# Optimization experiments

Measured on AMD Instinct MI355X. Metric: run time of the kernel, lower is better.

The kernel has to match this reference:

```python
import jax, jax.numpy as jnp
import numpy as np

T, H, F, E, K = 2048, 1024, 1024, 8, 2  # tokens, hidden, ffn, experts, top_k


def setup_inputs() -> dict:
    key = jax.random.key(0)
    k1, k2, k3, k4, k5 = jax.random.split(key, 5)
    hidden_states = jax.random.normal(k1, (T, H), dtype=jnp.float32)
    # router outputs: positive weights (renormalize=False in module, used as-is)
    topk_weights = jax.random.uniform(k2, (T, K), dtype=jnp.float32)
    topk_ids = jax.random.randint(k3, (T, K), 0, E, dtype=jnp.int32)
    # gate_up: (E, 2F, H) with first F rows = gate, last F rows = up
    gate_up_weight = jax.random.normal(k4, (E, 2 * F, H), dtype=jnp.float32) * 0.02
    # down: (E, H, F)
    down_weight = jax.random.normal(k5, (E, H, F), dtype=jnp.float32) * 0.02
    return {
        'hidden_states': hidden_states,
        'topk_weights': topk_weights,
        'topk_ids': topk_ids,
        'gate_up_weight': gate_up_weight,
        'down_weight': down_weight,
    }


def reference(hidden_states, topk_weights, topk_ids, gate_up_weight, down_weight):
    # Fused MoE: per selected expert, y = (silu(x@Wg^T) * (x@Wu^T)) @ Wd^T,
    # combined with router weights (renormalize=False).
    f = down_weight.shape[-1]
    # [T, E, 2F]: gate_up projection for every expert (dense ref for grouped GEMM)
    gu = jnp.einsum('th,eoh->teo', hidden_states, gate_up_weight)
    gate, up = gu[..., :f], gu[..., f:]
    act = jax.nn.silu(gate) * up                     # [T, E, F]
    y = jnp.einsum('tef,ehf->teh', act, down_weight)  # [T, E, H]
    # gather the top-k experts per token and combine
    y_sel = jnp.take_along_axis(y, topk_ids[:, :, None], axis=1)  # [T, K, H]
    out = jnp.sum(y_sel * topk_weights[:, :, None], axis=1)       # [T, H]
    return out.astype(hidden_states.dtype)
```

## Files before the change

kernel.cpp:

```cpp
#include <hip/hip_runtime.h>
#include <hip/hip_bf16.h>

#define T_TOK 2048
#define HID   1024
#define FF    1024
#define NEXP  8
#define TOPK  2
#define NPAIR (T_TOK*TOPK)

#define BM 128
#define BN 128
#define BK 32
#define MAX_MT 40
#define MAXROWS (MAX_MT*BM)

using bf16x8 = __attribute__((ext_vector_type(8))) __bf16;
using f32x4  = __attribute__((ext_vector_type(4))) float;

__device__ __forceinline__ unsigned short f2bf(float f) {
    unsigned int u = __float_as_uint(f);
    unsigned int r = (u + 0x7FFF + ((u >> 16) & 1)) >> 16;
    return (unsigned short)r;
}
__device__ __forceinline__ float bf2f(unsigned short s) {
    return __uint_as_float(((unsigned int)s) << 16);
}

__global__ void setup_kernel(const int* __restrict__ ids,
                             int* __restrict__ pair_pos,
                             int* __restrict__ meta) {
    __shared__ int cnt[NEXP], cnt2[NEXP], base[NEXP];
    int tid = threadIdx.x;
    if (tid < NEXP) { cnt[tid] = 0; cnt2[tid] = 0; }
    __syncthreads();
    for (int p = tid; p < NPAIR; p += 256) atomicAdd(&cnt[ids[p]], 1);
    __syncthreads();
    if (tid == 0) {
        int mt = 0;
        for (int e = 0; e < NEXP; e++) {
            meta[e] = mt;
            base[e] = mt * BM;
            mt += (cnt[e] + BM - 1) / BM;
        }
        meta[NEXP] = mt;
    }
    __syncthreads();
    for (int p = tid; p < NPAIR; p += 256) {
        int e = ids[p];
        int pos = base[e] + atomicAdd(&cnt2[e], 1);
        pair_pos[p] = pos;
    }
}

__global__ void cvt_bf16_kernel(const float* __restrict__ src,
                                unsigned short* __restrict__ dst, long n) {
    long i = ((long)blockIdx.x * blockDim.x + threadIdx.x) * 4;
    long stride = (long)gridDim.x * blockDim.x * 4;
    for (; i < n; i += stride) {
        float4 v = *(const float4*)(src + i);
        ushort4 o;
        o.x = f2bf(v.x); o.y = f2bf(v.y); o.z = f2bf(v.z); o.w = f2bf(v.w);
        *(ushort4*)(dst + i) = o;
    }
}

__global__ void gather_kernel(const float* __restrict__ hs,
                              const int* __restrict__ pair_pos,
                              unsigned short* __restrict__ A) {
    int p = blockIdx.x;
    int t = p >> 1;
    int pos = pair_pos[p];
    int c = threadIdx.x * 4;
    float4 v = *(const float4*)(hs + (long)t * HID + c);
    ushort4 o;
    o.x = f2bf(v.x); o.y = f2bf(v.y); o.z = f2bf(v.z); o.w = f2bf(v.w);
    *(ushort4*)(A + (long)pos * HID + c) = o;
}

__global__ __launch_bounds__(256)
void gemm_bt_moe(const unsigned short* __restrict__ A,
                 const unsigned short* __restrict__ B,
                 unsigned short* __restrict__ C,
                 const int* __restrict__ meta,
                 int K, int Ntot, long Bexp) {
    __shared__ unsigned short As[BM * BK];
    __shared__ unsigned short Bs[BN * BK];
    int bx = blockIdx.x, by = blockIdx.y;
    if (bx >= meta[NEXP]) return;
    int e = 0;
#pragma unroll
    for (int i = 1; i < NEXP; i++) if (bx >= meta[i]) e = i;

    long m0 = (long)bx * BM;
    long n0 = (long)by * BN;
    const unsigned short* Ab = A + m0 * K;
    const unsigned short* Bb = B + (long)e * Bexp + n0 * K;

    int tid = threadIdx.x, lane = tid & 63, wv = tid >> 6;
    const int qr8 = (lane >> 4) * 8;
    const int r = lane & 15;
    const int mw = (wv >> 1) * 64, nw = (wv & 1) * 64;

    f32x4 acc[4][4] = {};

    for (int k0 = 0; k0 < K; k0 += BK) {
        __syncthreads();
#pragma unroll
        for (int i = 0; i < 2; i++) {
            int chunk = i * 256 + tid;
            int row = chunk >> 2, cc = chunk & 3;
            const unsigned short* ga = Ab + (long)row * K + k0 + cc * 8;
            const unsigned short* gb = Bb + (long)row * K + k0 + cc * 8;
            unsigned short* la = &As[(i * 256 + wv * 64) * 8];
            unsigned short* lb = &Bs[(i * 256 + wv * 64) * 8];
            __builtin_amdgcn_global_load_lds((const __attribute__((address_space(1))) void*)(const void*)ga,
                                             (__attribute__((address_space(3))) void*)(void*)la, 16, 0, 0);
            __builtin_amdgcn_global_load_lds((const __attribute__((address_space(1))) void*)(const void*)gb,
                                             (__attribute__((address_space(3))) void*)(void*)lb, 16, 0, 0);
        }
        __syncthreads();

        bf16x8 a[4], b[4];
#pragma unroll
        for (int i = 0; i < 4; i++) {
            a[i] = *(const bf16x8*)&As[(mw + i * 16 + r) * BK + qr8];
            b[i] = *(const bf16x8*)&Bs[(nw + i * 16 + r) * BK + qr8];
        }
#pragma unroll
        for (int i = 0; i < 4; i++)
#pragma unroll
            for (int j = 0; j < 4; j++)
                acc[i][j] = __builtin_amdgcn_mfma_f32_16x16x32_bf16(a[i], b[j], acc[i][j], 0, 0, 0);
    }

#pragma unroll
    for (int i = 0; i < 4; i++) {
        int rowb = mw + i * 16 + (lane >> 4) * 4;
#pragma unroll
        for (int j = 0; j < 4; j++) {
            int col = nw + j * 16 + r;
#pragma unroll
            for (int reg = 0; reg < 4; reg++) {
                C[(m0 + rowb + reg) * (long)Ntot + n0 + col] = f2bf(acc[i][j][reg]);
            }
        }
    }
}

__global__ void silu_kernel(const unsigned short* __restrict__ gu,
                            unsigned short* __restrict__ act) {
    long idx = ((long)blockIdx.x * 256 + threadIdx.x) * 4;
    long row = idx >> 10;
    int f = (int)(idx & 1023);
    const unsigned short* gp = gu + row * (2 * FF) + f;
    ushort4 g = *(const ushort4*)gp;
    ushort4 u = *(const ushort4*)(gp + FF);
    ushort4 o;
    {
        float x = bf2f(g.x); o.x = f2bf(x / (1.f + __expf(-x)) * bf2f(u.x));
        float y = bf2f(g.y); o.y = f2bf(y / (1.f + __expf(-y)) * bf2f(u.y));
        float z = bf2f(g.z); o.z = f2bf(z / (1.f + __expf(-z)) * bf2f(u.z));
        float w = bf2f(g.w); o.w = f2bf(w / (1.f + __expf(-w)) * bf2f(u.w));
    }
    *(ushort4*)(act + row * FF + f) = o;
}

__global__ void combine_kernel(const unsigned short* __restrict__ y,
                               const float* __restrict__ tw,
                               const int* __restrict__ pair_pos,
                               float* __restrict__ out) {
    int t = blockIdx.x;
    int c = threadIdx.x * 4;
    int p0 = pair_pos[t * 2], p1 = pair_pos[t * 2 + 1];
    float w0 = tw[t * 2], w1 = tw[t * 2 + 1];
    ushort4 a = *(const ushort4*)(y + (long)p0 * HID + c);
    ushort4 b = *(const ushort4*)(y + (long)p1 * HID + c);
    float4 o;
    o.x = w0 * bf2f(a.x) + w1 * bf2f(b.x);
    o.y = w0 * bf2f(a.y) + w1 * bf2f(b.y);
    o.z = w0 * bf2f(a.z) + w1 * bf2f(b.z);
    o.w = w0 * bf2f(a.w) + w1 * bf2f(b.w);
    *(float4*)(out + (long)t * HID + c) = o;
}

extern "C" void kernel_launch(void* const* d_in, const int* in_sizes, int n_in,
                              void* d_out, int out_size, void* d_ws, size_t ws_size,
                              hipStream_t stream) {
    const float* hs  = (const float*)d_in[0];
    const float* tw  = (const float*)d_in[1];
    const int*   ids = (const int*)d_in[2];
    const float* wgu = (const float*)d_in[3];
    const float* wdn = (const float*)d_in[4];
    float* out = (float*)d_out;

    char* ws = (char*)d_ws;
    size_t off = 0;
    auto alloc = [&](size_t bytes) -> void* {
        void* p = ws + off;
        off += (bytes + 255) & ~(size_t)255;
        return p;
    };
    unsigned short* wgu_b = (unsigned short*)alloc((size_t)NEXP * 2 * FF * HID * 2);
    unsigned short* wdn_b = (unsigned short*)alloc((size_t)NEXP * HID * FF * 2);
    unsigned short* Abuf  = (unsigned short*)alloc((size_t)MAXROWS * HID * 2);
    unsigned short* gu    = (unsigned short*)alloc((size_t)MAXROWS * 2 * FF * 2);
    unsigned short* act   = (unsigned short*)alloc((size_t)MAXROWS * FF * 2);
    unsigned short* ybuf  = (unsigned short*)alloc((size_t)MAXROWS * HID * 2);
    int* pair_pos = (int*)alloc(NPAIR * 4);
    int* meta     = (int*)alloc(64);

    hipMemsetAsync(Abuf, 0, (size_t)MAXROWS * HID * 2, stream);

    setup_kernel<<<1, 256, 0, stream>>>(ids, pair_pos, meta);
    cvt_bf16_kernel<<<4096, 256, 0, stream>>>(wgu, wgu_b, (long)NEXP * 2 * FF * HID);
    cvt_bf16_kernel<<<2048, 256, 0, stream>>>(wdn, wdn_b, (long)NEXP * HID * FF);
    gather_kernel<<<NPAIR, 256, 0, stream>>>(hs, pair_pos, Abuf);

    gemm_bt_moe<<<dim3(MAX_MT, (2 * FF) / BN), 256, 0, stream>>>(
        Abuf, wgu_b, gu, meta, HID, 2 * FF, (long)(2 * FF) * HID);
    silu_kernel<<<MAXROWS, 256, 0, stream>>>(gu, act);
    gemm_bt_moe<<<dim3(MAX_MT, HID / BN), 256, 0, stream>>>(
        act, wdn_b, ybuf, meta, FF, HID, (long)HID * FF);
    combine_kernel<<<T_TOK, 256, 0, stream>>>(ybuf, tw, pair_pos, out);
}
```

Baseline: 236.4 us.

## Fuse SiLU and weighted combine into grouped GEMM epilogues, merge prep kernels

Weight conversion and token gather are merged into a single prep kernel, and gate/up rows are interleaved so each gate sits next to its up value. SiLU-gating then runs in the first GEMM epilogue through a lane shuffle. The down GEMM scatters router-weighted results into the fp32 output with atomics, which removes the silu and combine kernels and their intermediate buffers. The GEMM N tile shrinks to 64 to launch more blocks. This adds atomic contention on the output and an extra output memset, and float atomics make the summation order nondeterministic.

Result: no change. 241.1 us (+2.0%).

```diff
diff --git a/kernel.cpp b/kernel.cpp
--- a/kernel.cpp
+++ b/kernel.cpp
@@ -5,11 +5,9 @@
 #define HID   1024
 #define FF    1024
 #define NEXP  8
-#define TOPK  2
-#define NPAIR (T_TOK*TOPK)
+#define NPAIR 4096
 
 #define BM 128
-#define BN 128
 #define BK 32
 #define MAX_MT 40
 #define MAXROWS (MAX_MT*BM)
@@ -27,13 +25,17 @@
 }
 
 __global__ void setup_kernel(const int* __restrict__ ids,
+                             const float* __restrict__ tw,
                              int* __restrict__ pair_pos,
+                             int* __restrict__ row_tok,
+                             float* __restrict__ row_w,
                              int* __restrict__ meta) {
     __shared__ int cnt[NEXP], cnt2[NEXP], base[NEXP];
     int tid = threadIdx.x;
     if (tid < NEXP) { cnt[tid] = 0; cnt2[tid] = 0; }
     __syncthreads();
     for (int p = tid; p < NPAIR; p += 256) atomicAdd(&cnt[ids[p]], 1);
+    for (int i = tid; i < MAXROWS; i += 256) row_tok[i] = -1;
     __syncthreads();
     if (tid == 0) {
         int mt = 0;
@@ -49,42 +51,58 @@
         int e = ids[p];
         int pos = base[e] + atomicAdd(&cnt2[e], 1);
         pair_pos[p] = pos;
-    }
-}
-
-__global__ void cvt_bf16_kernel(const float* __restrict__ src,
-                                unsigned short* __restrict__ dst, long n) {
-    long i = ((long)blockIdx.x * blockDim.x + threadIdx.x) * 4;
-    long stride = (long)gridDim.x * blockDim.x * 4;
-    for (; i < n; i += stride) {
-        float4 v = *(const float4*)(src + i);
-        ushort4 o;
-        o.x = f2bf(v.x); o.y = f2bf(v.y); o.z = f2bf(v.z); o.w = f2bf(v.w);
-        *(ushort4*)(dst + i) = o;
-    }
-}
-
-__global__ void gather_kernel(const float* __restrict__ hs,
-                              const int* __restrict__ pair_pos,
-                              unsigned short* __restrict__ A) {
-    int p = blockIdx.x;
-    int t = p >> 1;
-    int pos = pair_pos[p];
+        row_tok[pos] = p >> 1;
+        row_w[pos] = tw[p];
+    }
+}
+
+#define NB_GU (NEXP*2*FF)
+#define NB_DN (NEXP*HID)
+__global__ void prep_kernel(const float* __restrict__ wgu,
+                            const float* __restrict__ wdn,
+                            const float* __restrict__ hs,
+                            const int* __restrict__ pair_pos,
+                            unsigned short* __restrict__ wgu_b,
+                            unsigned short* __restrict__ wdn_b,
+                            unsigned short* __restrict__ A) {
+    int b = blockIdx.x;
     int c = threadIdx.x * 4;
-    float4 v = *(const float4*)(hs + (long)t * HID + c);
+    const float* src;
+    unsigned short* dst;
+    if (b < NB_GU) {
+        int e = b >> 11;
+        int o = b & (2 * FF - 1);
+        int nr = (o < FF) ? (2 * o) : (2 * (o - FF) + 1);
+        src = wgu + (long)b * HID;
+        dst = wgu_b + ((long)e * 2 * FF + nr) * HID;
+    } else if (b < NB_GU + NB_DN) {
+        int rb = b - NB_GU;
+        src = wdn + (long)rb * FF;
+        dst = wdn_b + (long)rb * FF;
+    } else {
+        int p = b - (NB_GU + NB_DN);
+        int t = p >> 1;
+        src = hs + (long)t * HID;
+        dst = A + (long)pair_pos[p] * HID;
+    }
+    float4 v = *(const float4*)(src + c);
     ushort4 o;
     o.x = f2bf(v.x); o.y = f2bf(v.y); o.z = f2bf(v.z); o.w = f2bf(v.w);
-    *(ushort4*)(A + (long)pos * HID + c) = o;
-}
-
+    *(ushort4*)(dst + c) = o;
+}
+
+template<int BN_, int EPI>
 __global__ __launch_bounds__(256)
-void gemm_bt_moe(const unsigned short* __restrict__ A,
-                 const unsigned short* __restrict__ B,
-                 unsigned short* __restrict__ C,
-                 const int* __restrict__ meta,
-                 int K, int Ntot, long Bexp) {
+void gemm_moe(const unsigned short* __restrict__ A,
+              const unsigned short* __restrict__ B,
+              unsigned short* __restrict__ Cbf,
+              float* __restrict__ outf,
+              const int* __restrict__ meta,
+              const int* __restrict__ row_tok,
+              const float* __restrict__ row_w,
+              int K, int Ntot, long Bexp) {
     __shared__ unsigned short As[BM * BK];
-    __shared__ unsigned short Bs[BN * BK];
+    __shared__ unsigned short Bs[BN_ * BK];
     int bx = blockIdx.x, by = blockIdx.y;
     if (bx >= meta[NEXP]) return;
     int e = 0;
@@ -92,95 +110,96 @@
     for (int i = 1; i < NEXP; i++) if (bx >= meta[i]) e = i;
 
     long m0 = (long)bx * BM;
-    long n0 = (long)by * BN;
+    long n0 = (long)by * BN_;
     const unsigned short* Ab = A + m0 * K;
     const unsigned short* Bb = B + (long)e * Bexp + n0 * K;
 
     int tid = threadIdx.x, lane = tid & 63, wv = tid >> 6;
     const int qr8 = (lane >> 4) * 8;
     const int r = lane & 15;
-    const int mw = (wv >> 1) * 64, nw = (wv & 1) * 64;
-
-    f32x4 acc[4][4] = {};
+    const int quad = lane >> 4;
+    const int mw = (wv >> 1) * 64, nw = (wv & 1) * (BN_ / 2);
+    constexpr int NJ = BN_ / 32;
+
+    f32x4 acc[4][NJ] = {};
 
     for (int k0 = 0; k0 < K; k0 += BK) {
         __syncthreads();
 #pragma unroll
-        for (int i = 0; i < 2; i++) {
-            int chunk = i * 256 + tid;
-            int row = chunk >> 2, cc = chunk & 3;
-            const unsigned short* ga = Ab + (long)row * K + k0 + cc * 8;
-            const unsigned short* gb = Bb + (long)row * K + k0 + cc * 8;
-            unsigned short* la = &As[(i * 256 + wv * 64) * 8];
-            unsigned short* lb = &Bs[(i * 256 + wv * 64) * 8];
-            __builtin_amdgcn_global_load_lds((const __attribute__((address_space(1))) void*)(const void*)ga,
-                                             (__attribute__((address_space(3))) void*)(void*)la, 16, 0, 0);
-            __builtin_amdgcn_global_load_lds((const __attribute__((address_space(1))) void*)(const void*)gb,
-                                             (__attribute__((address_space(3))) void*)(void*)lb, 16, 0, 0);
+        for (int it = 0; it < 2 + BN_ / 64; it++) {
+            int chunk = it * 256 + tid;
+            const unsigned short* g;
+            unsigned short* l;
+            if (it < 2) {
+                int row = chunk >> 2, cc = chunk & 3;
+                g = Ab + (long)row * K + k0 + cc * 8;
+                l = &As[chunk * 8];
+            } else {
+                int cb = chunk - 512;
+                int row = cb >> 2, cc = cb & 3;
+                g = Bb + (long)row * K + k0 + cc * 8;
+                l = &Bs[cb * 8];
+            }
+            __builtin_amdgcn_global_load_lds(
+                (const __attribute__((address_space(1))) void*)(const void*)g,
+                (__attribute__((address_space(3))) void*)(void*)l, 16, 0, 0);
         }
         __syncthreads();
 
-        bf16x8 a[4], b[4];
+        bf16x8 a[4], b[NJ];
+#pragma unroll
+        for (int i = 0; i < 4; i++)
+            a[i] = *(const bf16x8*)&As[(mw + i * 16 + r) * BK + qr8];
+#pragma unroll
+        for (int j = 0; j < NJ; j++)
+            b[j] = *(const bf16x8*)&Bs[(nw + j * 16 + r) * BK + qr8];
+#pragma unroll
+        for (int i = 0; i < 4; i++)
+#pragma unroll
+            for (int j = 0; j < NJ; j++)
+                acc[i][j] = __builtin_amdgcn_mfma_f32_16x16x32_bf16(a[i], b[j], acc[i][j], 0, 0, 0);
+    }
+
+    if (EPI == 1) {
 #pragma unroll
         for (int i = 0; i < 4; i++) {
-            a[i] = *(const bf16x8*)&As[(mw + i * 16 + r) * BK + qr8];
-            b[i] = *(const bf16x8*)&Bs[(nw + i * 16 + r) * BK + qr8];
-        }
-#pragma unroll
-        for (int i = 0; i < 4; i++)
-#pragma unroll
-            for (int j = 0; j < 4; j++)
-                acc[i][j] = __builtin_amdgcn_mfma_f32_16x16x32_bf16(a[i], b[j], acc[i][j], 0, 0, 0);
-    }
-
-#pragma unroll
-    for (int i = 0; i < 4; i++) {
-        int rowb = mw + i * 16 + (lane >> 4) * 4;
-#pragma unroll
-        for (int j = 0; j < 4; j++) {
-            int col = nw + j * 16 + r;
+            long rowb = m0 + mw + i * 16 + quad * 4;
+#pragma unroll
+            for (int j = 0; j < NJ; j++) {
+                int n = (int)n0 + nw + j * 16 + r;
+#pragma unroll
+                for (int reg = 0; reg < 4; reg++) {
+                    float v = acc[i][j][reg];
+                    float o = __shfl_xor(v, 1);
+                    if (!(r & 1)) {
+                        float g = v, u = o;
+                        float s = g / (1.f + __expf(-g)) * u;
+                        Cbf[(rowb + reg) * (long)(Ntot / 2) + (n >> 1)] = f2bf(s);
+                    }
+                }
+            }
+        }
+    } else {
+#pragma unroll
+        for (int i = 0; i < 4; i++) {
+            int rowb = (int)m0 + mw + i * 16 + quad * 4;
+            int tk[4]; float w[4];
 #pragma unroll
             for (int reg = 0; reg < 4; reg++) {
-                C[(m0 + rowb + reg) * (long)Ntot + n0 + col] = f2bf(acc[i][j][reg]);
-            }
-        }
-    }
-}
-
-__global__ void silu_kernel(const unsigned short* __restrict__ gu,
-                            unsigned short* __restrict__ act) {
-    long idx = ((long)blockIdx.x * 256 + threadIdx.x) * 4;
-    long row = idx >> 10;
-    int f = (int)(idx & 1023);
-    const unsigned short* gp = gu + row * (2 * FF) + f;
-    ushort4 g = *(const ushort4*)gp;
-    ushort4 u = *(const ushort4*)(gp + FF);
-    ushort4 o;
-    {
-        float x = bf2f(g.x); o.x = f2bf(x / (1.f + __expf(-x)) * bf2f(u.x));
-        float y = bf2f(g.y); o.y = f2bf(y / (1.f + __expf(-y)) * bf2f(u.y));
-        float z = bf2f(g.z); o.z = f2bf(z / (1.f + __expf(-z)) * bf2f(u.z));
-        float w = bf2f(g.w); o.w = f2bf(w / (1.f + __expf(-w)) * bf2f(u.w));
-    }
-    *(ushort4*)(act + row * FF + f) = o;
-}
-
-__global__ void combine_kernel(const unsigned short* __restrict__ y,
-                               const float* __restrict__ tw,
-                               const int* __restrict__ pair_pos,
-                               float* __restrict__ out) {
-    int t = blockIdx.x;
-    int c = threadIdx.x * 4;
-    int p0 = pair_pos[t * 2], p1 = pair_pos[t * 2 + 1];
-    float w0 = tw[t * 2], w1 = tw[t * 2 + 1];
-    ushort4 a = *(const ushort4*)(y + (long)p0 * HID + c);
-    ushort4 b = *(const ushort4*)(y + (long)p1 * HID + c);
-    float4 o;
-    o.x = w0 * bf2f(a.x) + w1 * bf2f(b.x);
-    o.y = w0 * bf2f(a.y) + w1 * bf2f(b.y);
-    o.z = w0 * bf2f(a.z) + w1 * bf2f(b.z);
-    o.w = w0 * bf2f(a.w) + w1 * bf2f(b.w);
-    *(float4*)(out + (long)t * HID + c) = o;
+                tk[reg] = row_tok[rowb + reg];
+                w[reg] = row_w[rowb + reg];
+            }
+#pragma unroll
+            for (int j = 0; j < NJ; j++) {
+                int n = (int)n0 + nw + j * 16 + r;
+#pragma unroll
+                for (int reg = 0; reg < 4; reg++) {
+                    if (tk[reg] >= 0)
+                        atomicAdd(outf + (long)tk[reg] * HID + n, w[reg] * acc[i][j][reg]);
+                }
+            }
+        }
+    }
 }
 
 extern "C" void kernel_launch(void* const* d_in, const int* in_sizes, int n_in,
@@ -203,23 +222,24 @@
     unsigned short* wgu_b = (unsigned short*)alloc((size_t)NEXP * 2 * FF * HID * 2);
     unsigned short* wdn_b = (unsigned short*)alloc((size_t)NEXP * HID * FF * 2);
     unsigned short* Abuf  = (unsigned short*)alloc((size_t)MAXROWS * HID * 2);
-    unsigned short* gu    = (unsigned short*)alloc((size_t)MAXROWS * 2 * FF * 2);
     unsigned short* act   = (unsigned short*)alloc((size_t)MAXROWS * FF * 2);
-    unsigned short* ybuf  = (unsigned short*)alloc((size_t)MAXROWS * HID * 2);
-    int* pair_pos = (int*)alloc(NPAIR * 4);
-    int* meta     = (int*)alloc(64);
+    int*   pair_pos = (int*)alloc(NPAIR * 4);
+    int*   row_tok  = (int*)alloc(MAXROWS * 4);
+    float* row_w    = (float*)alloc(MAXROWS * 4);
+    int*   meta     = (int*)alloc(64);
 
     hipMemsetAsync(Abuf, 0, (size_t)MAXROWS * HID * 2, stream);
-
-    setup_kernel<<<1, 256, 0, stream>>>(ids, pair_pos, meta);
-    cvt_bf16_kernel<<<4096, 256, 0, stream>>>(wgu, wgu_b, (long)NEXP * 2 * FF * HID);
-    cvt_bf16_kernel<<<2048, 256, 0, stream>>>(wdn, wdn_b, (long)NEXP * HID * FF);
-    gather_kernel<<<NPAIR, 256, 0, stream>>>(hs, pair_pos, Abuf);
-
-    gemm_bt_moe<<<dim3(MAX_MT, (2 * FF) / BN), 256, 0, stream>>>(
-        Abuf, wgu_b, gu, meta, HID, 2 * FF, (long)(2 * FF) * HID);
-    silu_kernel<<<MAXROWS, 256, 0, stream>>>(gu, act);
-    gemm_bt_moe<<<dim3(MAX_MT, HID / BN), 256, 0, stream>>>(
-        act, wdn_b, ybuf, meta, FF, HID, (long)HID * FF);
-    combine_kernel<<<T_TOK, 256, 0, stream>>>(ybuf, tw, pair_pos, out);
-}
+    hipMemsetAsync(out, 0, (size_t)T_TOK * HID * 4, stream);
+
+    setup_kernel<<<1, 256, 0, stream>>>(ids, tw, pair_pos, row_tok, row_w, meta);
+    prep_kernel<<<NB_GU + NB_DN + NPAIR, 256, 0, stream>>>(
+        wgu, wdn, hs, pair_pos, wgu_b, wdn_b, Abuf);
+
+    gemm_moe<64, 1><<<dim3(MAX_MT, (2 * FF) / 64), 256, 0, stream>>>(
+        Abuf, wgu_b, act, nullptr, meta, nullptr, nullptr,
+        HID, 2 * FF, (long)(2 * FF) * HID);
+
+    gemm_moe<64, 2><<<dim3(MAX_MT, HID / 64), 256, 0, stream>>>(
+        act, wdn_b, nullptr, out, meta, row_tok, row_w,
+        FF, HID, (long)HID * FF);
+}
```
